# Performance work log

Hardware: AMD Instinct MI355X
Metric: run time of the kernel (lower is better)

Reference implementation:

```python
import jax, jax.numpy as jnp
import numpy as np

B, T, E, H = 8, 2048, 1024, 64


def setup_inputs() -> dict:
    key = jax.random.key(0)
    kx, kq, kk, kv = jax.random.split(key, 4)
    x = jax.random.normal(kx, (B, T, E), dtype=jnp.float32)
    # nn.Linear(E, H, bias=False) weights, stored as (E, H) so y = x @ W
    scale = 0.02
    Wq = jax.random.normal(kq, (E, H), dtype=jnp.float32) * scale
    Wk = jax.random.normal(kk, (E, H), dtype=jnp.float32) * scale
    Wv = jax.random.normal(kv, (E, H), dtype=jnp.float32) * scale
    return {"x": x, "Wq": Wq, "Wk": Wk, "Wv": Wv}


def reference(x, Wq, Wk, Wv):
    # q, k, v: (B, T, H)
    q = x @ Wq
    k = x @ Wk
    v = x @ Wv
    # scores: (B, T, T)
    scores = jnp.einsum("btd,bsd->bts", q, k) / jnp.sqrt(jnp.asarray(H, q.dtype))
    # NOTE: the original module applies softmax over dim=0 (the batch dim).
    # With mask=None and is_decoder=False this is the only softmax applied.
    p = jax.nn.softmax(scores, axis=0)
    # output: (B, T, H)
    return jnp.einsum("bts,bsd->btd", p, v)
```

## Files before the change

### kernel.cpp

```cpp
#include <hip/hip_runtime.h>
#include <hip/hip_bf16.h>


typedef __attribute__((ext_vector_type(4))) float f32x4;
typedef __attribute__((ext_vector_type(4))) float float4_t;
typedef __attribute__((ext_vector_type(8))) short short8;
typedef __attribute__((ext_vector_type(4))) unsigned uint4_t;
typedef __attribute__((ext_vector_type(2))) unsigned uint2_t;

#define MFMA32(a, b, c) __builtin_amdgcn_mfma_f32_16x16x32_bf16(a, b, c, 0, 0, 0)

__device__ __forceinline__ short f2bf(float f) {
  unsigned u = __builtin_bit_cast(unsigned, f);
  unsigned r = (u + 0x7FFFu + ((u >> 16) & 1u)) >> 16;
  return (short)r;
}

__device__ __forceinline__ unsigned cvt_pk_bf16(float lo, float hi) {
  unsigned r;
  asm volatile("v_cvt_pk_bf16_f32 %0, %1, %2" : "=v"(r) : "v"(lo), "v"(hi));
  return r;
}

__device__ __forceinline__ void gload16(const short* g, short* l) {
  __builtin_amdgcn_global_load_lds(
      (const __attribute__((address_space(1))) unsigned*)g,
      (__attribute__((address_space(3))) unsigned*)l, 16, 0, 0);
}

__global__ __launch_bounds__(256) void wprep_kernel(
    const float* __restrict__ Wq, const float* __restrict__ Wk,
    const float* __restrict__ Wv, short* __restrict__ Wtb) {
  int lin = blockIdx.x * 256 + threadIdx.x;
  int n = lin & 63;
  int k8 = (lin >> 6) & 127;
  int wi = lin >> 13;
  const float* W = (wi == 0) ? Wq : (wi == 1) ? Wk : Wv;
  short* dst = Wtb + wi * 65536 + n * 1024 + k8 * 8;
#pragma unroll
  for (int i = 0; i < 8; i++) dst[i] = f2bf(W[(k8 * 8 + i) * 64 + n]);
}

__device__ __forceinline__ void proj_stage(const float* __restrict__ x,
                                           const short* __restrict__ Wtb,
                                           short* dst, int m0, int k0, int w, int l) {
  const int g = l >> 4, lr = l & 15;
  if (w < 4) {
#pragma unroll
    for (int i = 0; i < 5; i++) {
      int u = w * 5 + i;
      if (u < 8) {
        int xwr = u >> 1, h = u & 1;
        const float* src = x + (size_t)(m0 + xwr * 16 + lr) * 1024 + k0 + g * 8 + h * 4;
        gload16((const short*)src, dst + u * 512);
      } else {
        int cf = u - 8;
        const short* src = Wtb + (cf * 16 + lr) * 1024 + k0 + g * 8;
        gload16(src, dst + u * 512);
      }
    }
  }
}

__device__ __forceinline__ void proj_compute(const short* __restrict__ ldsb,
                                             f32x4 (&acc)[6], int wr, int wc, int l) {
  f32x4 fa = *(const f32x4*)&ldsb[(wr * 2 + 0) * 512 + l * 8];
  f32x4 fb = *(const f32x4*)&ldsb[(wr * 2 + 1) * 512 + l * 8];
  uint4_t u_;
  u_[0] = cvt_pk_bf16(fa[0], fa[1]);
  u_[1] = cvt_pk_bf16(fa[2], fa[3]);
  u_[2] = cvt_pk_bf16(fb[0], fb[1]);
  u_[3] = cvt_pk_bf16(fb[2], fb[3]);
  short8 a = __builtin_bit_cast(short8, u_);
#pragma unroll
  for (int nf = 0; nf < 6; nf++) {
    int cf = wc * 6 + nf;
    short8 bfrag = *(const short8*)&ldsb[(8 + cf) * 512 + l * 8];
    acc[nf] = MFMA32(a, bfrag, acc[nf]);
  }
}

__global__ __launch_bounds__(512) void proj_kernel(
    const float* __restrict__ x, const short* __restrict__ Wtb,
    short* __restrict__ qb, short* __restrict__ kvb) {
  __shared__ __align__(16) short lds[3 * 20 * 512];
  const int tid = threadIdx.x;
  const int l = tid & 63, w = tid >> 6;
  const int g = l >> 4, lr = l & 15;
  const int wr = w & 3, wc = w >> 2;
  const int m0 = blockIdx.x * 64;

  f32x4 acc[6];
#pragma unroll
  for (int i = 0; i < 6; i++) acc[i] = (f32x4){0.f, 0.f, 0.f, 0.f};

  short* bA = lds;
  short* bB = lds + 10240;
  short* bC = lds + 20480;
  proj_stage(x, Wtb, bA, m0, 0, w, l);
  proj_stage(x, Wtb, bB, m0, 32, w, l);

  for (int I = 0; I < 31; I++) {
    asm volatile("s_waitcnt vmcnt(5)" ::: "memory");
    __builtin_amdgcn_s_barrier();
    __builtin_amdgcn_sched_barrier(0);
    if (I + 2 < 32) proj_stage(x, Wtb, bC, m0, (I + 2) * 32, w, l);
    proj_compute(bA, acc, wr, wc, l);
    short* t = bA; bA = bB; bB = bC; bC = t;
  }
  asm volatile("s_waitcnt vmcnt(0)" ::: "memory");
  __builtin_amdgcn_s_barrier();
  __builtin_amdgcn_sched_barrier(0);
  proj_compute(bA, acc, wr, wc, l);

#pragma unroll
  for (int nf = 0; nf < 6; nf++) {
    int colg0 = wc * 96 + nf * 16;
    int wi = colg0 >> 6;
    int d = (colg0 & 63) + lr;
    float scale = (wi == 0) ? 0.18033688f : 1.0f;
#pragma unroll
    for (int r = 0; r < 4; r++) {
      int row = m0 + wr * 16 + g * 4 + r;
      int b = row >> 11, t = row & 2047;
      short bv = f2bf(acc[nf][r] * scale);
      if (wi == 0) {
        int idx = (((b * 128 + (t >> 4)) * 2 + (d >> 5)) * 64 +
                   ((((d >> 3) & 3) << 4) | (t & 15))) * 8 + (d & 7);
        qb[idx] = bv;
      } else if (wi == 1) {
        int u = (b << 2) | (((t >> 4) & 1) << 1) | (d >> 5);
        int idx = (((t >> 5) * 64 + u) << 9) +
                  ((((((d >> 3) & 3) << 4)) | (t & 15)) << 3) + (d & 7);
        kvb[idx] = bv;
      } else {
        int u = 32 + (b << 2) + (d >> 4);
        int idx = (((t >> 5) * 64 + u) << 9) +
                  (((((t >> 2) & 3) << 4) | (d & 15)) << 3) + (((t >> 4) & 1) << 2) + (t & 3);
        kvb[idx] = bv;
      }
    }
  }
}

__device__ __forceinline__ void stage_step(const short* __restrict__ kvb,
                                           short* lds_buf, int w, int l, int W) {
#pragma unroll
  for (int i = 0; i < 8; i++) {
    int u = w * 8 + i;
    const short* src = kvb + (((size_t)W * 64 + u) << 9) + l * 8;
    gload16(src, lds_buf + u * 512);
  }
}

__global__ __launch_bounds__(512, 2) void attn_kernel(
    const short* __restrict__ qb, const short* __restrict__ kvb,
    short* __restrict__ partial) {
  __shared__ __align__(16) short lds[2][64 * 512];
  const int tid = threadIdx.x;
  const int l = tid & 63, w = tid >> 6;
  const int tt = w >> 1, dh = w & 1;
  const int lin = blockIdx.x;
  const int sc = lin & 7;
  const int tblk = lin >> 3;
  const int tb16 = tblk * 4 + tt;

  short8 qf[8][2];
#pragma unroll
  for (int b = 0; b < 8; b++)
#pragma unroll
    for (int ks = 0; ks < 2; ks++)
      qf[b][ks] = *(const short8*)&qb[(size_t)((b * 128 + tb16) * 2 + ks) * 512 + l * 8];

  f32x4 oacc[8][2];
#pragma unroll
  for (int b = 0; b < 8; b++)
#pragma unroll
    for (int n = 0; n < 2; n++) oacc[b][n] = (f32x4){0.f, 0.f, 0.f, 0.f};

  stage_step(kvb, &lds[0][0], w, l, sc * 8);

  for (int it = 0; it < 8; it++) {
    __syncthreads();
    if (it + 1 < 8) stage_step(kvb, &lds[(it + 1) & 1][0], w, l, sc * 8 + it + 1);
    const short* ldsc = &lds[it & 1][0];

    uint2_t plo[8], phi[8];
#pragma unroll
    for (int sf = 0; sf < 2; sf++) {
      f32x4 S[8];
      __builtin_amdgcn_s_setprio(1);
#pragma unroll
      for (int b = 0; b < 8; b++) {
        short8 kf0 = *(const short8*)&ldsc[(b * 4 + sf * 2 + 0) * 512 + l * 8];
        short8 kf1 = *(const short8*)&ldsc[(b * 4 + sf * 2 + 1) * 512 + l * 8];
        f32x4 s = (f32x4){0.f, 0.f, 0.f, 0.f};
        s = MFMA32(kf0, qf[b][0], s);
        s = MFMA32(kf1, qf[b][1], s);
        S[b] = s;
      }
      __builtin_amdgcn_s_setprio(0);
#pragma unroll
      for (int r = 0; r < 4; r++) {
        float den = 0.f;
#pragma unroll
        for (int b = 0; b < 8; b++) {
          float e = __builtin_amdgcn_exp2f(S[b][r]);
          S[b][r] = e;
          den += e;
        }
        float inv = __builtin_amdgcn_rcpf(den);
#pragma unroll
        for (int b = 0; b < 8; b++) S[b][r] *= inv;
      }
#pragma unroll
      for (int b = 0; b < 8; b++) {
        uint2_t pw;
        pw[0] = cvt_pk_bf16(S[b][0], S[b][1]);
        pw[1] = cvt_pk_bf16(S[b][2], S[b][3]);
        if (sf == 0) plo[b] = pw; else phi[b] = pw;
      }
    }
    __builtin_amdgcn_s_setprio(1);
#pragma unroll
    for (int b = 0; b < 8; b++) {
      uint4_t pu;
      pu[0] = plo[b][0]; pu[1] = plo[b][1]; pu[2] = phi[b][0]; pu[3] = phi[b][1];
      short8 pbv = __builtin_bit_cast(short8, pu);
      short8 vf0 = *(const short8*)&ldsc[(32 + b * 4 + dh * 2 + 0) * 512 + l * 8];
      short8 vf1 = *(const short8*)&ldsc[(32 + b * 4 + dh * 2 + 1) * 512 + l * 8];
      oacc[b][0] = MFMA32(vf0, pbv, oacc[b][0]);
      oacc[b][1] = MFMA32(vf1, pbv, oacc[b][1]);
    }
    __builtin_amdgcn_s_setprio(0);
  }

  uint2_t* pout = (uint2_t*)partial;
#pragma unroll
  for (int b = 0; b < 8; b++)
#pragma unroll
    for (int n = 0; n < 2; n++) {
      int df = dh * 2 + n;
      uint2_t pk;
      pk[0] = cvt_pk_bf16(oacc[b][n][0], oacc[b][n][1]);
      pk[1] = cvt_pk_bf16(oacc[b][n][2], oacc[b][n][3]);
      __builtin_nontemporal_store(
          pk, &pout[(size_t)(((sc * 8 + b) * 128 + tb16) * 4 + df) * 64 + l]);
    }
}

__global__ __launch_bounds__(256) void reduce_kernel(const short* __restrict__ partial,
                                                     float* __restrict__ out) {
  int i = blockIdx.x * 256 + threadIdx.x;
  const uint2_t* p = (const uint2_t*)partial;
  float4_t a = (float4_t){0.f, 0.f, 0.f, 0.f};
  for (int sc = 0; sc < 8; sc++) {
    uint2_t v = __builtin_nontemporal_load(&p[(size_t)sc * 262144 + i]);
    a[0] += __builtin_bit_cast(float, v[0] << 16);
    a[1] += __builtin_bit_cast(float, v[0] & 0xFFFF0000u);
    a[2] += __builtin_bit_cast(float, v[1] << 16);
    a[3] += __builtin_bit_cast(float, v[1] & 0xFFFF0000u);
  }
  int b = i >> 15;
  int r1 = i & 32767;
  int tb16 = r1 >> 8;
  int r2 = r1 & 255;
  int df = r2 >> 6;
  int ll = r2 & 63;
  int gg = ll >> 4, lrr = ll & 15;
  *(float4_t*)&out[(size_t)(b * 2048 + tb16 * 16 + lrr) * 64 + df * 16 + gg * 4] = a;
}

extern "C" void kernel_launch(void* const* d_in, const int* in_sizes, int n_in,
                              void* d_out, int out_size, void* d_ws, size_t ws_size,
                              hipStream_t stream) {
  const float* x = (const float*)d_in[0];
  const float* Wq = (const float*)d_in[1];
  const float* Wk = (const float*)d_in[2];
  const float* Wv = (const float*)d_in[3];
  float* out = (float*)d_out;

  char* ws = (char*)d_ws;
  short* qb = (short*)ws;
  short* kvb = qb + 16384 * 64;
  short* partial = kvb + 2 * 16384 * 64;
  short* Wtb = partial + 8ull * 262144 * 4;

  wprep_kernel<<<96, 256, 0, stream>>>(Wq, Wk, Wv, Wtb);
  proj_kernel<<<256, 512, 0, stream>>>(x, Wtb, qb, kvb);
  attn_kernel<<<256, 512, 0, stream>>>(qb, kvb, partial);
  reduce_kernel<<<1024, 256, 0, stream>>>(partial, out);
}
```

Measured before the change: 62.97 us.

## Load x directly into registers and stage only weights through LDS

New measurement: 80.93 us. 28.5% more time.

```diff
diff --git a/kernel.cpp b/kernel.cpp
--- a/kernel.cpp
+++ b/kernel.cpp
@@ -41,77 +41,101 @@
   for (int i = 0; i < 8; i++) dst[i] = f2bf(W[(k8 * 8 + i) * 64 + n]);
 }
 
-__device__ __forceinline__ void proj_stage(const float* __restrict__ x,
-                                           const short* __restrict__ Wtb,
-                                           short* dst, int m0, int k0, int w, int l) {
+__device__ __forceinline__ void stage_W(const short* __restrict__ Wtb,
+                                        short* dst, int k0, int w, int l) {
   const int g = l >> 4, lr = l & 15;
-  if (w < 4) {
-#pragma unroll
-    for (int i = 0; i < 5; i++) {
-      int u = w * 5 + i;
-      if (u < 8) {
-        int xwr = u >> 1, h = u & 1;
-        const float* src = x + (size_t)(m0 + xwr * 16 + lr) * 1024 + k0 + g * 8 + h * 4;
-        gload16((const short*)src, dst + u * 512);
-      } else {
-        int cf = u - 8;
-        const short* src = Wtb + (cf * 16 + lr) * 1024 + k0 + g * 8;
-        gload16(src, dst + u * 512);
-      }
-    }
-  }
+#pragma unroll
+  for (int i = 0; i < 3; i++) {
+    int u = w * 3 + i;
+    int cf = u >> 1, ks = u & 1;
+    const short* src = Wtb + (cf * 16 + lr) * 1024 + k0 + ks * 32 + g * 8;
+    gload16(src, dst + u * 512);
+  }
+}
+
+__device__ __forceinline__ void load_x(const float* __restrict__ xbase, int k0,
+                                       f32x4 (&xb)[4]) {
+  xb[0] = __builtin_nontemporal_load((const float4_t*)(xbase + k0));
+  xb[1] = __builtin_nontemporal_load((const float4_t*)(xbase + k0 + 4));
+  xb[2] = __builtin_nontemporal_load((const float4_t*)(xbase + k0 + 32));
+  xb[3] = __builtin_nontemporal_load((const float4_t*)(xbase + k0 + 36));
 }
 
 __device__ __forceinline__ void proj_compute(const short* __restrict__ ldsb,
-                                             f32x4 (&acc)[6], int wr, int wc, int l) {
-  f32x4 fa = *(const f32x4*)&ldsb[(wr * 2 + 0) * 512 + l * 8];
-  f32x4 fb = *(const f32x4*)&ldsb[(wr * 2 + 1) * 512 + l * 8];
-  uint4_t u_;
-  u_[0] = cvt_pk_bf16(fa[0], fa[1]);
-  u_[1] = cvt_pk_bf16(fa[2], fa[3]);
-  u_[2] = cvt_pk_bf16(fb[0], fb[1]);
-  u_[3] = cvt_pk_bf16(fb[2], fb[3]);
-  short8 a = __builtin_bit_cast(short8, u_);
-#pragma unroll
-  for (int nf = 0; nf < 6; nf++) {
-    int cf = wc * 6 + nf;
-    short8 bfrag = *(const short8*)&ldsb[(8 + cf) * 512 + l * 8];
-    acc[nf] = MFMA32(a, bfrag, acc[nf]);
-  }
-}
-
-__global__ __launch_bounds__(512) void proj_kernel(
+                                             const f32x4 (&xb)[4],
+                                             f32x4 (&acc)[6], int wc, int l) {
+#pragma unroll
+  for (int ks = 0; ks < 2; ks++) {
+    uint4_t u_;
+    u_[0] = cvt_pk_bf16(xb[ks * 2][0], xb[ks * 2][1]);
+    u_[1] = cvt_pk_bf16(xb[ks * 2][2], xb[ks * 2][3]);
+    u_[2] = cvt_pk_bf16(xb[ks * 2 + 1][0], xb[ks * 2 + 1][1]);
+    u_[3] = cvt_pk_bf16(xb[ks * 2 + 1][2], xb[ks * 2 + 1][3]);
+    short8 a = __builtin_bit_cast(short8, u_);
+#pragma unroll
+    for (int nf = 0; nf < 6; nf++) {
+      int cf = wc * 6 + nf;
+      short8 bfrag = *(const short8*)&ldsb[(cf * 2 + ks) * 512 + l * 8];
+      acc[nf] = MFMA32(a, bfrag, acc[nf]);
+    }
+  }
+}
+
+template <int I>
+__device__ __forceinline__ void proj_step(const float* __restrict__ xbase,
+                                          const short* __restrict__ Wtb, short* lds,
+                                          f32x4 (&xb0)[4], f32x4 (&xb1)[4],
+                                          f32x4 (&acc)[6], int w, int wc, int l) {
+  constexpr int NW = (I == 15) ? 4 : 7;
+  __builtin_amdgcn_sched_barrier(0);
+  asm volatile("s_waitcnt vmcnt(%0)" ::"n"(NW) : "memory");
+  __builtin_amdgcn_s_barrier();
+  __builtin_amdgcn_sched_barrier(0);
+  if constexpr (I + 2 < 16) stage_W(Wtb, lds + ((I + 2) % 3) * 12288, (I + 2) * 64, w, l);
+  if constexpr (I + 1 < 16) {
+    if constexpr ((I & 1) == 0) load_x(xbase, (I + 1) * 64, xb1);
+    else                        load_x(xbase, (I + 1) * 64, xb0);
+  }
+  if constexpr ((I & 1) == 0) proj_compute(lds + (I % 3) * 12288, xb0, acc, wc, l);
+  else                        proj_compute(lds + (I % 3) * 12288, xb1, acc, wc, l);
+}
+
+__global__ __launch_bounds__(512, 4) void proj_kernel(
     const float* __restrict__ x, const short* __restrict__ Wtb,
     short* __restrict__ qb, short* __restrict__ kvb) {
-  __shared__ __align__(16) short lds[3 * 20 * 512];
+  __shared__ __align__(16) short lds[3 * 24 * 512];
   const int tid = threadIdx.x;
   const int l = tid & 63, w = tid >> 6;
   const int g = l >> 4, lr = l & 15;
   const int wr = w & 3, wc = w >> 2;
   const int m0 = blockIdx.x * 64;
+  const float* xbase = x + (size_t)(m0 + wr * 16 + lr) * 1024 + g * 8;
 
   f32x4 acc[6];
 #pragma unroll
   for (int i = 0; i < 6; i++) acc[i] = (f32x4){0.f, 0.f, 0.f, 0.f};
 
-  short* bA = lds;
-  short* bB = lds + 10240;
-  short* bC = lds + 20480;
-  proj_stage(x, Wtb, bA, m0, 0, w, l);
-  proj_stage(x, Wtb, bB, m0, 32, w, l);
-
-  for (int I = 0; I < 31; I++) {
-    asm volatile("s_waitcnt vmcnt(5)" ::: "memory");
-    __builtin_amdgcn_s_barrier();
-    __builtin_amdgcn_sched_barrier(0);
-    if (I + 2 < 32) proj_stage(x, Wtb, bC, m0, (I + 2) * 32, w, l);
-    proj_compute(bA, acc, wr, wc, l);
-    short* t = bA; bA = bB; bB = bC; bC = t;
-  }
-  asm volatile("s_waitcnt vmcnt(0)" ::: "memory");
-  __builtin_amdgcn_s_barrier();
-  __builtin_amdgcn_sched_barrier(0);
-  proj_compute(bA, acc, wr, wc, l);
+  f32x4 xb0[4], xb1[4];
+  stage_W(Wtb, lds, 0, w, l);
+  stage_W(Wtb, lds + 12288, 64, w, l);
+  load_x(xbase, 0, xb0);
+
+  proj_step<0>(xbase, Wtb, lds, xb0, xb1, acc, w, wc, l);
+  proj_step<1>(xbase, Wtb, lds, xb0, xb1, acc, w, wc, l);
+  proj_step<2>(xbase, Wtb, lds, xb0, xb1, acc, w, wc, l);
+  proj_step<3>(xbase, Wtb, lds, xb0, xb1, acc, w, wc, l);
+  proj_step<4>(xbase, Wtb, lds, xb0, xb1, acc, w, wc, l);
+  proj_step<5>(xbase, Wtb, lds, xb0, xb1, acc, w, wc, l);
+  proj_step<6>(xbase, Wtb, lds, xb0, xb1, acc, w, wc, l);
+  proj_step<7>(xbase, Wtb, lds, xb0, xb1, acc, w, wc, l);
+  proj_step<8>(xbase, Wtb, lds, xb0, xb1, acc, w, wc, l);
+  proj_step<9>(xbase, Wtb, lds, xb0, xb1, acc, w, wc, l);
+  proj_step<10>(xbase, Wtb, lds, xb0, xb1, acc, w, wc, l);
+  proj_step<11>(xbase, Wtb, lds, xb0, xb1, acc, w, wc, l);
+  proj_step<12>(xbase, Wtb, lds, xb0, xb1, acc, w, wc, l);
+  proj_step<13>(xbase, Wtb, lds, xb0, xb1, acc, w, wc, l);
+  proj_step<14>(xbase, Wtb, lds, xb0, xb1, acc, w, wc, l);
+  proj_step<15>(xbase, Wtb, lds, xb0, xb1, acc, w, wc, l);
 
 #pragma unroll
   for (int nf = 0; nf < 6; nf++) {
```
